# Performance work log

Measured on AMD Instinct MI355X. Metric: run time of the kernel, lower is better.

The kernel has to match this reference:

```python
import jax, jax.numpy as jnp
import numpy as np

NEG_INF = -1e10  # matches torch's -10000000000.0 fill


def setup_inputs() -> dict:
    key = jax.random.key(0)
    k1, k2, k3, k4, k5, k6 = jax.random.split(key, 6)
    B, N, D_IN, D_HID, D_OUT = 8, 2048, 512, 512, 512
    H = jax.random.normal(k1, (B, N, D_IN), dtype=jnp.float32)
    bias = jax.random.normal(k2, (B, N, N), dtype=jnp.float32)
    mask = jax.random.randint(k3, (B, N, N), 0, 2, dtype=jnp.int32)
    s = 1.0 / np.sqrt(D_IN)
    Wq = jax.random.normal(k4, (D_IN, D_HID), dtype=jnp.float32) * s
    Wk = jax.random.normal(k5, (D_IN, D_HID), dtype=jnp.float32) * s
    Wv = jax.random.normal(k6, (D_IN, D_OUT), dtype=jnp.float32) * s
    return {"H": H, "bias": bias, "mask": mask, "Wq": Wq, "Wk": Wk, "Wv": Wv}


def reference(H, bias, mask, Wq, Wk, Wv):
    # Q,K: [B,N,d_hid], V: [B,N,d_out]
    Q = H @ Wq
    K = H @ Wk
    V = H @ Wv
    d = Q.shape[-1]
    scale = 1.0 / jnp.sqrt(jnp.asarray(d, dtype=Q.dtype))
    # scores: [B,N,N]; scale, add bias, then fill masked-out entries
    scores = jnp.einsum("bnd,bmd->bnm", Q, K) * scale + bias
    scores = jnp.where(mask == 0, jnp.asarray(NEG_INF, scores.dtype), scores)
    atn = jax.nn.softmax(scores, axis=-1)
    return jnp.einsum("bnm,bmo->bno", atn, V)
```

## Files before the change

kernel.cpp:

```cpp
#include <hip/hip_runtime.h>
#include <hip/hip_bf16.h>

typedef __attribute__((ext_vector_type(8))) short short8;
typedef __attribute__((ext_vector_type(4))) float floatx4;
typedef __attribute__((ext_vector_type(4))) int intx4;
typedef __attribute__((ext_vector_type(4))) unsigned short ushortx4;

#define NB 8
#define NN 2048
#define DD 512

__device__ __forceinline__ unsigned short f2bf(float f) {
  union { float f; unsigned int u; } v; v.f = f;
  unsigned int u = v.u;
  return (unsigned short)((u + 0x7fffu + ((u >> 16) & 1u)) >> 16);
}
__device__ __forceinline__ float bf2f(unsigned short s) {
  union { unsigned int u; float f; } v; v.u = ((unsigned int)s) << 16;
  return v.f;
}

typedef __attribute__((address_space(3))) unsigned short lds_us;
typedef __attribute__((address_space(1))) const unsigned short glb_us;

__device__ __forceinline__ void ld_lds16(const unsigned short* g, unsigned short* l) {
  __builtin_amdgcn_global_load_lds((glb_us*)g, (lds_us*)l, 16, 0, 0);
}

__global__ __launch_bounds__(256) void mha_cvtH(const float* __restrict__ H,
                                                unsigned short* __restrict__ Hb, int n8) {
  int i = blockIdx.x * 256 + threadIdx.x;
  if (i >= n8) return;
  const float4* src = (const float4*)H;
  float4 a = src[2 * i], b = src[2 * i + 1];
  short8 o;
  o[0] = (short)f2bf(a.x); o[1] = (short)f2bf(a.y); o[2] = (short)f2bf(a.z); o[3] = (short)f2bf(a.w);
  o[4] = (short)f2bf(b.x); o[5] = (short)f2bf(b.y); o[6] = (short)f2bf(b.z); o[7] = (short)f2bf(b.w);
  *(short8*)(Hb + 8 * i) = o;
}

__global__ __launch_bounds__(256) void mha_prep(const floatx4* __restrict__ bias,
                                                const intx4* __restrict__ mask,
                                                ushortx4* __restrict__ bm) {
  int i = blockIdx.x * 256 + threadIdx.x;
  floatx4 bv = __builtin_nontemporal_load(&bias[i]);
  intx4 mv = __builtin_nontemporal_load(&mask[i]);
  const unsigned short NINF = 0xFF80;
  ushortx4 o;
  o.x = mv.x ? f2bf(bv.x) : NINF;
  o.y = mv.y ? f2bf(bv.y) : NINF;
  o.z = mv.z ? f2bf(bv.z) : NINF;
  o.w = mv.w ? f2bf(bv.w) : NINF;
  __builtin_nontemporal_store(o, &bm[i]);
}

__global__ __launch_bounds__(256) void mha_tW(const float* __restrict__ Wq, const float* __restrict__ Wk,
                                              const float* __restrict__ Wv,
                                              unsigned short* __restrict__ Wqt, unsigned short* __restrict__ Wkt,
                                              unsigned short* __restrict__ Wvt) {
  const float* W = (blockIdx.z == 0) ? Wq : (blockIdx.z == 1) ? Wk : Wv;
  unsigned short* Wt = (blockIdx.z == 0) ? Wqt : (blockIdx.z == 1) ? Wkt : Wvt;
  __shared__ float tile[32][33];
  int d0 = blockIdx.x * 32, k0 = blockIdx.y * 32;
  int t = threadIdx.x, r = t >> 3, c4 = (t & 7) * 4;
  float4 v = *(const float4*)(W + (size_t)(k0 + r) * DD + d0 + c4);
  tile[r][c4] = v.x; tile[r][c4 + 1] = v.y; tile[r][c4 + 2] = v.z; tile[r][c4 + 3] = v.w;
  __syncthreads();
  union { unsigned short s[4]; uint2 v; } u;
  u.s[0] = f2bf(tile[c4][r]);     u.s[1] = f2bf(tile[c4 + 1][r]);
  u.s[2] = f2bf(tile[c4 + 2][r]); u.s[3] = f2bf(tile[c4 + 3][r]);
  *(uint2*)(Wt + (size_t)(d0 + r) * DD + k0 + c4) = u.v;
}

__global__ __launch_bounds__(256) void mha_tV(const unsigned short* __restrict__ Vr,
                                              unsigned short* __restrict__ Vt) {
  int b = blockIdx.z;
  int d0 = blockIdx.x * 32, n0 = blockIdx.y * 32;
  __shared__ unsigned short tile[32][34];
  int t = threadIdx.x, r = t >> 3, c4 = (t & 7) * 4;
  union { uint2 v; unsigned short s[4]; } u;
  u.v = *(const uint2*)(Vr + ((size_t)b * NN + n0 + r) * DD + d0 + c4);
  tile[r][c4] = u.s[0]; tile[r][c4 + 1] = u.s[1]; tile[r][c4 + 2] = u.s[2]; tile[r][c4 + 3] = u.s[3];
  __syncthreads();
  union { unsigned short s[4]; uint2 v; } o;
  o.s[0] = tile[c4][r]; o.s[1] = tile[c4 + 1][r]; o.s[2] = tile[c4 + 2][r]; o.s[3] = tile[c4 + 3][r];
  *(uint2*)(Vt + ((size_t)b * DD + d0 + r) * NN + n0 + c4) = o.v;
}

__device__ __forceinline__ void stage_tile_async(const unsigned short* __restrict__ g, int ld,
                                                 unsigned short* s, int t) {
#pragma unroll
  for (int h = 0; h < 2; ++h) {
    int c = t + h * 256;
    int r = c >> 2, p = c & 3;
    int seg = (p - (r >> 1)) & 3;
    ld_lds16(g + (size_t)r * ld + seg * 8, s + c * 8);
  }
}

__device__ __forceinline__ void mfma_step(const unsigned short* As, const unsigned short* Bs,
                                          int wr, int wc, int quad, int lr, floatx4 acc[4][4]) {
  short8 a[4], b[4];
#pragma unroll
  for (int i = 0; i < 4; ++i) {
    int ra = wr * 64 + i * 16 + lr;
    int rb = wc * 64 + i * 16 + lr;
    a[i] = *(const short8*)(As + ra * 32 + ((quad + (ra >> 1)) & 3) * 8);
    b[i] = *(const short8*)(Bs + rb * 32 + ((quad + (rb >> 1)) & 3) * 8);
  }
#pragma unroll
  for (int i = 0; i < 4; ++i)
#pragma unroll
    for (int j = 0; j < 4; ++j)
      acc[i][j] = __builtin_amdgcn_mfma_f32_16x16x32_bf16(a[i], b[j], acc[i][j], 0, 0, 0);
}

__global__ __launch_bounds__(256) void mha_proj(const unsigned short* __restrict__ Hb,
                                                const unsigned short* __restrict__ Wqt,
                                                const unsigned short* __restrict__ Wkt,
                                                const unsigned short* __restrict__ Wvt,
                                                unsigned short* __restrict__ Qb,
                                                unsigned short* __restrict__ Kb,
                                                unsigned short* __restrict__ Vr) {
  const unsigned short* Wt = (blockIdx.z == 0) ? Wqt : (blockIdx.z == 1) ? Wkt : Wvt;
  unsigned short* dst = (blockIdx.z == 0) ? Qb : (blockIdx.z == 1) ? Kb : Vr;
  __shared__ unsigned short As[128 * 32], Bs[128 * 32];
  int t = threadIdx.x, wave = t >> 6, lane = t & 63, quad = lane >> 4, lr = lane & 15;
  int wr = wave >> 1, wc = wave & 1;
  int m0 = blockIdx.y * 128, n0 = blockIdx.x * 128;
  floatx4 acc[4][4] = {};
  for (int k0 = 0; k0 < DD; k0 += 32) {
    __syncthreads();
    stage_tile_async(Hb + (size_t)m0 * DD + k0, DD, As, t);
    stage_tile_async(Wt + (size_t)n0 * DD + k0, DD, Bs, t);
    __syncthreads();
    mfma_step(As, Bs, wr, wc, quad, lr, acc);
  }
#pragma unroll
  for (int i = 0; i < 4; ++i)
#pragma unroll
    for (int j = 0; j < 4; ++j)
#pragma unroll
      for (int r = 0; r < 4; ++r) {
        int row = m0 + wr * 64 + i * 16 + quad * 4 + r;
        int col = n0 + wc * 64 + j * 16 + lr;
        dst[(size_t)row * DD + col] = f2bf(acc[i][j][r]);
      }
}

__global__ __launch_bounds__(256) void mha_scores(const unsigned short* __restrict__ Qb,
                                                  const unsigned short* __restrict__ Kb,
                                                  unsigned short* __restrict__ bmE,
                                                  float* __restrict__ l) {
  __shared__ unsigned short As[128 * 32], Bs[128 * 32], Bm[128 * 128];
  int b = blockIdx.z;
  int i0 = blockIdx.y * 128;
  int j0 = blockIdx.x * 128;
  int t = threadIdx.x, wave = t >> 6, lane = t & 63, quad = lane >> 4, lr = lane & 15;
  int wr = wave >> 1, wc = wave & 1;
  const unsigned short* Q = Qb + (size_t)b * NN * DD;
  const unsigned short* K = Kb + (size_t)b * NN * DD;
  unsigned short* bm = bmE + (size_t)b * NN * NN;
  const float scale = 0.04419417382415922f;

  floatx4 acc[4][4] = {};
  for (int kidx = 0; kidx < 16; ++kidx) {
    int k0 = kidx * 32;
    __syncthreads();
    stage_tile_async(Q + (size_t)i0 * DD + k0, DD, As, t);
    stage_tile_async(K + (size_t)j0 * DD + k0, DD, Bs, t);
    if (kidx < 8) {
      int c = kidx * 256 + t;
      int row = c >> 4, phys = c & 15;
      int s = (phys - row) & 15;
      ld_lds16(bm + (size_t)(i0 + row) * NN + j0 + s * 8, Bm + c * 8);
    }
    __syncthreads();
    mfma_step(As, Bs, wr, wc, quad, lr, acc);
  }

  float rs[4][4] = {};
#pragma unroll
  for (int i = 0; i < 4; ++i) {
#pragma unroll
    for (int j = 0; j < 4; ++j) {
#pragma unroll
      for (int r = 0; r < 4; ++r) {
        int row_l = wr * 64 + i * 16 + quad * 4 + r;
        int col_l = wc * 64 + j * 16 + lr;
        int sseg = col_l >> 3;
        float bi = bf2f(Bm[(row_l * 16 + ((sseg + row_l) & 15)) * 8 + (col_l & 7)]);
        float sv = acc[i][j][r] * scale + bi - 16.0f;
        float e = __expf(sv);
        unsigned short eb = f2bf(e);
        __builtin_nontemporal_store(eb, &bm[(size_t)(i0 + row_l) * NN + j0 + col_l]);
        rs[i][r] += bf2f(eb);
      }
    }
  }
#pragma unroll
  for (int i = 0; i < 4; ++i)
#pragma unroll
    for (int r = 0; r < 4; ++r) {
      float v = rs[i][r];
      v += __shfl_xor(v, 1);
      v += __shfl_xor(v, 2);
      v += __shfl_xor(v, 4);
      v += __shfl_xor(v, 8);
      if (lr == 0) {
        int row = i0 + wr * 64 + i * 16 + quad * 4 + r;
        atomicAdd(&l[b * NN + row], v);
      }
    }
}

__global__ __launch_bounds__(256) void mha_pv(const unsigned short* __restrict__ E,
                                              const unsigned short* __restrict__ Vt,
                                              const float* __restrict__ l,
                                              float* __restrict__ out) {
  int b = blockIdx.z;
  int i0 = blockIdx.y * 128;
  int c0 = blockIdx.x * 128;
  __shared__ unsigned short As[128 * 32], Bs[128 * 32];
  int t = threadIdx.x, wave = t >> 6, lane = t & 63, quad = lane >> 4, lr = lane & 15;
  int wr = wave >> 1, wc = wave & 1;
  const unsigned short* Eb = E + (size_t)b * NN * NN;
  const unsigned short* Vb = Vt + (size_t)b * DD * NN;
  floatx4 acc[4][4] = {};
  for (int k0 = 0; k0 < NN; k0 += 32) {
    __syncthreads();
    stage_tile_async(Eb + (size_t)i0 * NN + k0, NN, As, t);
    stage_tile_async(Vb + (size_t)c0 * NN + k0, NN, Bs, t);
    __syncthreads();
    mfma_step(As, Bs, wr, wc, quad, lr, acc);
  }
#pragma unroll
  for (int i = 0; i < 4; ++i)
#pragma unroll
    for (int r = 0; r < 4; ++r) {
      int row = i0 + wr * 64 + i * 16 + quad * 4 + r;
      float linv = 1.0f / l[b * NN + row];
#pragma unroll
      for (int j = 0; j < 4; ++j) {
        int col = c0 + wc * 64 + j * 16 + lr;
        __builtin_nontemporal_store(acc[i][j][r] * linv,
                                    &out[((size_t)b * NN + row) * DD + col]);
      }
    }
}

extern "C" void kernel_launch(void* const* d_in, const int* in_sizes, int n_in,
                              void* d_out, int out_size, void* d_ws, size_t ws_size,
                              hipStream_t stream) {
  const float* H = (const float*)d_in[0];
  const float* bias = (const float*)d_in[1];
  const int* mask = (const int*)d_in[2];
  const float* Wq = (const float*)d_in[3];
  const float* Wk = (const float*)d_in[4];
  const float* Wv = (const float*)d_in[5];
  float* out = (float*)d_out;
  char* ws = (char*)d_ws;

  const size_t SZ_QKV = (size_t)NB * NN * DD * 2;
  const size_t SZ_W = (size_t)DD * DD * 2;
  unsigned short* Qb = (unsigned short*)(ws);
  unsigned short* Kb = (unsigned short*)(ws + SZ_QKV);
  unsigned short* Vt = (unsigned short*)(ws + 2 * SZ_QKV);
  float* l = (float*)(ws + 3 * SZ_QKV);
  char* base2 = ws + 3 * SZ_QKV + (((size_t)NB * NN * 4 + 255) & ~255ULL);
  unsigned short* bmE = (unsigned short*)(base2);
  unsigned short* Hb = (unsigned short*)(base2);
  unsigned short* Wqt = (unsigned short*)(base2 + SZ_QKV);
  unsigned short* Wkt = (unsigned short*)(base2 + SZ_QKV + SZ_W);
  unsigned short* Wvt = (unsigned short*)(base2 + SZ_QKV + 2 * SZ_W);
  unsigned short* Vr = (unsigned short*)(base2 + SZ_QKV + 3 * SZ_W);

  (void)hipMemsetAsync(l, 0, (size_t)NB * NN * 4, stream);
  mha_cvtH<<<dim3((NB * NN * DD / 8) / 256), 256, 0, stream>>>(H, Hb, NB * NN * DD / 8);
  mha_tW<<<dim3(DD / 32, DD / 32, 3), 256, 0, stream>>>(Wq, Wk, Wv, Wqt, Wkt, Wvt);
  mha_proj<<<dim3(DD / 128, NB * NN / 128, 3), 256, 0, stream>>>(Hb, Wqt, Wkt, Wvt, Qb, Kb, Vr);
  mha_tV<<<dim3(DD / 32, NN / 32, NB), 256, 0, stream>>>(Vr, Vt);
  mha_prep<<<dim3((NB * NN * NN / 4) / 256), 256, 0, stream>>>((const floatx4*)bias,
                                                               (const intx4*)mask, (ushortx4*)bmE);
  mha_scores<<<dim3(NN / 128, NN / 128, NB), 256, 0, stream>>>(Qb, Kb, bmE, l);
  mha_pv<<<dim3(DD / 128, NN / 128, NB), 256, 0, stream>>>(bmE, Vt, l, out);
}
```

Baseline: 496.2 us.

## Fuse scores and PV into a single flash-style attention kernel

```diff
diff --git a/kernel.cpp b/kernel.cpp
--- a/kernel.cpp
+++ b/kernel.cpp
@@ -148,104 +148,157 @@
       }
 }
 
-__global__ __launch_bounds__(256) void mha_scores(const unsigned short* __restrict__ Qb,
-                                                  const unsigned short* __restrict__ Kb,
-                                                  unsigned short* __restrict__ bmE,
-                                                  float* __restrict__ l) {
-  __shared__ unsigned short As[128 * 32], Bs[128 * 32], Bm[128 * 128];
-  int b = blockIdx.z;
-  int i0 = blockIdx.y * 128;
-  int j0 = blockIdx.x * 128;
-  int t = threadIdx.x, wave = t >> 6, lane = t & 63, quad = lane >> 4, lr = lane & 15;
-  int wr = wave >> 1, wc = wave & 1;
+__global__ __launch_bounds__(512) void mha_attn(const unsigned short* __restrict__ Qb,
+                                                const unsigned short* __restrict__ Kb,
+                                                const unsigned short* __restrict__ Vtb,
+                                                const unsigned short* __restrict__ bmE,
+                                                float* __restrict__ out) {
+  __shared__ unsigned short KV[2][16384];
+  __shared__ unsigned short Ps[64 * 128];
+  __shared__ unsigned short Bm[64 * 128];
+  __shared__ float ls[64];
+
+  const int b = blockIdx.x;
+  const int i0 = blockIdx.y * 64;
+  const int t = threadIdx.x;
+  const int wave = t >> 6, lane = t & 63, quad = lane >> 4, lr = lane & 15;
+  const int wi = wave & 3;
+  const int wj = wave >> 2;
+  const float scale = 0.04419417382415922f;
+
   const unsigned short* Q = Qb + (size_t)b * NN * DD;
   const unsigned short* K = Kb + (size_t)b * NN * DD;
-  unsigned short* bm = bmE + (size_t)b * NN * NN;
-  const float scale = 0.04419417382415922f;
-
-  floatx4 acc[4][4] = {};
-  for (int kidx = 0; kidx < 16; ++kidx) {
-    int k0 = kidx * 32;
-    __syncthreads();
-    stage_tile_async(Q + (size_t)i0 * DD + k0, DD, As, t);
-    stage_tile_async(K + (size_t)j0 * DD + k0, DD, Bs, t);
-    if (kidx < 8) {
-      int c = kidx * 256 + t;
-      int row = c >> 4, phys = c & 15;
-      int s = (phys - row) & 15;
-      ld_lds16(bm + (size_t)(i0 + row) * NN + j0 + s * 8, Bm + c * 8);
+  const unsigned short* V = Vtb + (size_t)b * DD * NN;
+  const unsigned short* bm = bmE + (size_t)b * NN * NN;
+
+  if (t < 64) ls[t] = 0.0f;
+
+  short8 q[16];
+#pragma unroll
+  for (int kc = 0; kc < 16; ++kc)
+    q[kc] = *(const short8*)(Q + (size_t)(i0 + wi * 16 + lr) * DD + kc * 32 + quad * 8);
+
+  floatx4 acc_o[4][4] = {};
+  float rs[4] = {0.f, 0.f, 0.f, 0.f};
+
+  const int krow = t >> 2, kphys = t & 3;
+  const int kseg = (kphys - (krow >> 1)) & 3;
+
+#pragma unroll
+  for (int h = 0; h < 4; ++h)
+    ld_lds16(K + (size_t)krow * DD + h * 32 + kseg * 8, KV[0] + h * 4096 + t * 8);
+#pragma unroll
+  for (int h = 0; h < 2; ++h) {
+    int c = t + h * 512, row = c >> 4, phys = c & 15, seg = (phys - row) & 15;
+    ld_lds16(bm + (size_t)(i0 + row) * NN + seg * 8, Bm + c * 8);
+  }
+  __syncthreads();
+
+  for (int tt = 0; tt < 16; ++tt) {
+    const int j0 = tt * 128;
+    floatx4 acc_s[4] = {};
+
+#pragma unroll
+    for (int s = 0; s < 4; ++s) {
+      if (s < 3) {
+#pragma unroll
+        for (int h = 0; h < 4; ++h)
+          ld_lds16(K + (size_t)(j0 + krow) * DD + (s + 1) * 128 + h * 32 + kseg * 8,
+                   KV[(s + 1) & 1] + h * 4096 + t * 8);
+      } else {
+#pragma unroll
+        for (int h = 0; h < 4; ++h) {
+          int c = t + h * 512, row = c >> 2, phys = c & 3, seg = (phys - (row >> 1)) & 3;
+          ld_lds16(V + (size_t)row * NN + j0 + seg * 8, KV[0] + c * 8);
+        }
+      }
+      const unsigned short* Ks = KV[s & 1];
+#pragma unroll
+      for (int kc = 0; kc < 4; ++kc) {
+#pragma unroll
+        for (int jt = 0; jt < 4; ++jt) {
+          int rb = wj * 64 + jt * 16 + lr;
+          short8 bf = *(const short8*)(Ks + kc * 4096 + rb * 32 + ((quad + (rb >> 1)) & 3) * 8);
+          acc_s[jt] = __builtin_amdgcn_mfma_f32_16x16x32_bf16(q[s * 4 + kc], bf, acc_s[jt], 0, 0, 0);
+        }
+      }
+      if (s == 3) {
+#pragma unroll
+        for (int jt = 0; jt < 4; ++jt) {
+          int col = wj * 64 + jt * 16 + lr;
+#pragma unroll
+          for (int rr = 0; rr < 4; ++rr) {
+            int row = wi * 16 + quad * 4 + rr;
+            float bi = bf2f(Bm[row * 128 + ((((col >> 3) + row) & 15) << 3) + (col & 7)]);
+            float e = __expf(acc_s[jt][rr] * scale + bi - 16.0f);
+            unsigned short eb = f2bf(e);
+            rs[rr] += bf2f(eb);
+            Ps[row * 128 + (col ^ ((row & 7) << 3))] = eb;
+          }
+        }
+      }
+      __syncthreads();
     }
-    __syncthreads();
-    mfma_step(As, Bs, wr, wc, quad, lr, acc);
-  }
-
-  float rs[4][4] = {};
-#pragma unroll
-  for (int i = 0; i < 4; ++i) {
-#pragma unroll
-    for (int j = 0; j < 4; ++j) {
-#pragma unroll
-      for (int r = 0; r < 4; ++r) {
-        int row_l = wr * 64 + i * 16 + quad * 4 + r;
-        int col_l = wc * 64 + j * 16 + lr;
-        int sseg = col_l >> 3;
-        float bi = bf2f(Bm[(row_l * 16 + ((sseg + row_l) & 15)) * 8 + (col_l & 7)]);
-        float sv = acc[i][j][r] * scale + bi - 16.0f;
-        float e = __expf(sv);
-        unsigned short eb = f2bf(e);
-        __builtin_nontemporal_store(eb, &bm[(size_t)(i0 + row_l) * NN + j0 + col_l]);
-        rs[i][r] += bf2f(eb);
-      }
+
+#pragma unroll
+    for (int jc = 0; jc < 4; ++jc) {
+      if (jc < 3) {
+#pragma unroll
+        for (int h = 0; h < 4; ++h) {
+          int c = t + h * 512, row = c >> 2, phys = c & 3, seg = (phys - (row >> 1)) & 3;
+          ld_lds16(V + (size_t)row * NN + j0 + (jc + 1) * 32 + seg * 8, KV[(jc + 1) & 1] + c * 8);
+        }
+      } else if (tt < 15) {
+#pragma unroll
+        for (int h = 0; h < 4; ++h)
+          ld_lds16(K + (size_t)(j0 + 128 + krow) * DD + h * 32 + kseg * 8,
+                   KV[0] + h * 4096 + t * 8);
+#pragma unroll
+        for (int h = 0; h < 2; ++h) {
+          int c = t + h * 512, row = c >> 4, phys = c & 15, seg = (phys - row) & 15;
+          ld_lds16(bm + (size_t)(i0 + row) * NN + j0 + 128 + seg * 8, Bm + c * 8);
+        }
+      }
+      const unsigned short* Vs = KV[jc & 1];
+      short8 pa[4];
+#pragma unroll
+      for (int it = 0; it < 4; ++it)
+        pa[it] = *(const short8*)(Ps + (it * 16 + lr) * 128 +
+                                  ((jc * 32 + quad * 8) ^ ((lr & 7) << 3)));
+#pragma unroll
+      for (int dt = 0; dt < 4; ++dt) {
+        int rb = wave * 64 + dt * 16 + lr;
+        short8 bf = *(const short8*)(Vs + rb * 32 + ((quad + (rb >> 1)) & 3) * 8);
+#pragma unroll
+        for (int it = 0; it < 4; ++it)
+          acc_o[it][dt] = __builtin_amdgcn_mfma_f32_16x16x32_bf16(pa[it], bf, acc_o[it][dt], 0, 0, 0);
+      }
+      __syncthreads();
     }
   }
-#pragma unroll
-  for (int i = 0; i < 4; ++i)
-#pragma unroll
-    for (int r = 0; r < 4; ++r) {
-      float v = rs[i][r];
-      v += __shfl_xor(v, 1);
-      v += __shfl_xor(v, 2);
-      v += __shfl_xor(v, 4);
-      v += __shfl_xor(v, 8);
-      if (lr == 0) {
-        int row = i0 + wr * 64 + i * 16 + quad * 4 + r;
-        atomicAdd(&l[b * NN + row], v);
-      }
-    }
-}
-
-__global__ __launch_bounds__(256) void mha_pv(const unsigned short* __restrict__ E,
-                                              const unsigned short* __restrict__ Vt,
-                                              const float* __restrict__ l,
-                                              float* __restrict__ out) {
-  int b = blockIdx.z;
-  int i0 = blockIdx.y * 128;
-  int c0 = blockIdx.x * 128;
-  __shared__ unsigned short As[128 * 32], Bs[128 * 32];
-  int t = threadIdx.x, wave = t >> 6, lane = t & 63, quad = lane >> 4, lr = lane & 15;
-  int wr = wave >> 1, wc = wave & 1;
-  const unsigned short* Eb = E + (size_t)b * NN * NN;
-  const unsigned short* Vb = Vt + (size_t)b * DD * NN;
-  floatx4 acc[4][4] = {};
-  for (int k0 = 0; k0 < NN; k0 += 32) {
-    __syncthreads();
-    stage_tile_async(Eb + (size_t)i0 * NN + k0, NN, As, t);
-    stage_tile_async(Vb + (size_t)c0 * NN + k0, NN, Bs, t);
-    __syncthreads();
-    mfma_step(As, Bs, wr, wc, quad, lr, acc);
-  }
-#pragma unroll
-  for (int i = 0; i < 4; ++i)
-#pragma unroll
-    for (int r = 0; r < 4; ++r) {
-      int row = i0 + wr * 64 + i * 16 + quad * 4 + r;
-      float linv = 1.0f / l[b * NN + row];
-#pragma unroll
-      for (int j = 0; j < 4; ++j) {
-        int col = c0 + wc * 64 + j * 16 + lr;
-        __builtin_nontemporal_store(acc[i][j][r] * linv,
-                                    &out[((size_t)b * NN + row) * DD + col]);
-      }
+
+#pragma unroll
+  for (int rr = 0; rr < 4; ++rr) {
+    float v = rs[rr];
+    v += __shfl_xor(v, 1);
+    v += __shfl_xor(v, 2);
+    v += __shfl_xor(v, 4);
+    v += __shfl_xor(v, 8);
+    if (lr == 0) atomicAdd(&ls[wi * 16 + quad * 4 + rr], v);
+  }
+  __syncthreads();
+
+  float* ob = out + ((size_t)b * NN + i0) * DD;
+#pragma unroll
+  for (int it = 0; it < 4; ++it)
+#pragma unroll
+    for (int rr = 0; rr < 4; ++rr) {
+      int row = it * 16 + quad * 4 + rr;
+      float linv = 1.0f / ls[row];
+#pragma unroll
+      for (int dt = 0; dt < 4; ++dt)
+        __builtin_nontemporal_store(acc_o[it][dt][rr] * linv,
+                                    &ob[(size_t)row * DD + wave * 64 + dt * 16 + lr]);
     }
 }
 
@@ -266,8 +319,7 @@
   unsigned short* Qb = (unsigned short*)(ws);
   unsigned short* Kb = (unsigned short*)(ws + SZ_QKV);
   unsigned short* Vt = (unsigned short*)(ws + 2 * SZ_QKV);
-  float* l = (float*)(ws + 3 * SZ_QKV);
-  char* base2 = ws + 3 * SZ_QKV + (((size_t)NB * NN * 4 + 255) & ~255ULL);
+  char* base2 = ws + 3 * SZ_QKV;
   unsigned short* bmE = (unsigned short*)(base2);
   unsigned short* Hb = (unsigned short*)(base2);
   unsigned short* Wqt = (unsigned short*)(base2 + SZ_QKV);
@@ -275,13 +327,11 @@
   unsigned short* Wvt = (unsigned short*)(base2 + SZ_QKV + 2 * SZ_W);
   unsigned short* Vr = (unsigned short*)(base2 + SZ_QKV + 3 * SZ_W);
 
-  (void)hipMemsetAsync(l, 0, (size_t)NB * NN * 4, stream);
   mha_cvtH<<<dim3((NB * NN * DD / 8) / 256), 256, 0, stream>>>(H, Hb, NB * NN * DD / 8);
   mha_tW<<<dim3(DD / 32, DD / 32, 3), 256, 0, stream>>>(Wq, Wk, Wv, Wqt, Wkt, Wvt);
   mha_proj<<<dim3(DD / 128, NB * NN / 128, 3), 256, 0, stream>>>(Hb, Wqt, Wkt, Wvt, Qb, Kb, Vr);
   mha_tV<<<dim3(DD / 32, NN / 32, NB), 256, 0, stream>>>(Vr, Vt);
   mha_prep<<<dim3((NB * NN * NN / 4) / 256), 256, 0, stream>>>((const floatx4*)bias,
                                                                (const intx4*)mask, (ushortx4*)bmE);
-  mha_scores<<<dim3(NN / 128, NN / 128, NB), 256, 0, stream>>>(Qb, Kb, bmE, l);
-  mha_pv<<<dim3(DD / 128, NN / 128, NB), 256, 0, stream>>>(bmE, Vt, l, out);
-}
+  mha_attn<<<dim3(NB, NN / 64), 512, 0, stream>>>(Qb, Kb, Vt, bmE, out);
+}
```

New measurement: 471.8 us. 4.9% less time.
